# Performance work log

Hardware: AMD Instinct MI355X
Metric: run time of the kernel (lower is better)

The kernel has to match this reference:

```python
import jax, jax.numpy as jnp
import numpy as np

B, T, H, W = 8, 10, 128, 128
WIDTH, NL = 64, 4
MT, MH, MW = 4, 8, 8
H_PRED = 5
MIN_STD = 1e-4


def setup_inputs() -> dict:
    key = jax.random.key(0)
    ks = jax.random.split(key, 12)
    scale = 1.0 / (WIDTH * WIDTH)
    return {
        "frames": jax.random.uniform(ks[0], (B, T, H, W), dtype=jnp.float32),
        "times": jax.random.uniform(ks[1], (B, T), dtype=jnp.float32),
        # lift: Conv3d(c_in=2 -> width, k=1)
        "lift_w": jax.random.normal(ks[2], (WIDTH, 2), dtype=jnp.float32) * 0.5,
        "lift_b": jnp.zeros((WIDTH,), jnp.float32),
        # spectral weights: (layer, quadrant, in, out, mt, mh, mw, re/im)
        "spec_w": jax.random.uniform(ks[3], (NL, 4, WIDTH, WIDTH, MT, MH, MW, 2), dtype=jnp.float32) * scale,
        # skip 1x1 Conv3d per layer
        "skip_w": jax.random.normal(ks[4], (NL, WIDTH, WIDTH), dtype=jnp.float32) * (1.0 / np.sqrt(WIDTH)),
        "skip_b": jnp.zeros((NL, WIDTH), jnp.float32),
        # temporal aggregation Conv3d kernel (h_ctx,1,1): (out, in, T)
        "agg_w": jax.random.normal(ks[5], (WIDTH, WIDTH, T), dtype=jnp.float32) * (1.0 / np.sqrt(WIDTH * T)),
        "agg_b": jnp.zeros((WIDTH,), jnp.float32),
        "fc1_w": jax.random.normal(ks[6], (WIDTH + 2, 128), dtype=jnp.float32) * (1.0 / np.sqrt(WIDTH + 2)),
        "fc1_b": jnp.zeros((128,), jnp.float32),
        "fc2_w": jax.random.normal(ks[7], (128, 2 * H_PRED), dtype=jnp.float32) * (1.0 / np.sqrt(128)),
        "fc2_b": jnp.zeros((2 * H_PRED,), jnp.float32),
    }


def _spectral_conv(x, wl):
    # x: (B, C, T, H, W); wl: (4, C, C, MT, MH, MW, 2) real/imag
    w = wl[..., 0] + 1j * wl[..., 1]  # (4, C, C, MT, MH, MW) complex
    x_ft = jnp.fft.rfftn(x, axes=(-3, -2, -1), norm="ortho")  # (B,C,T,H,W//2+1)
    Bc, C, Tt, Hh, Wf = x_ft.shape

    def mul(blk, wq):
        return jnp.einsum("bixyz,ioxyz->boxyz", blk, wq)

    out_ft = jnp.zeros((Bc, C, Tt, Hh, Wf), dtype=x_ft.dtype)
    out_ft = out_ft.at[:, :, :MT, :MH, :MW].set(mul(x_ft[:, :, :MT, :MH, :MW], w[0]))
    out_ft = out_ft.at[:, :, :MT, Hh - MH:, :MW].set(mul(x_ft[:, :, :MT, Hh - MH:, :MW], w[1]))
    out_ft = out_ft.at[:, :, Tt - MT:, :MH, :MW].set(mul(x_ft[:, :, Tt - MT:, :MH, :MW], w[2]))
    out_ft = out_ft.at[:, :, Tt - MT:, Hh - MH:, :MW].set(mul(x_ft[:, :, Tt - MT:, Hh - MH:, :MW], w[3]))
    return jnp.fft.irfftn(out_ft, s=(Tt, x.shape[-2], x.shape[-1]), axes=(-3, -2, -1), norm="ortho")


def reference(frames, times, lift_w, lift_b, spec_w, skip_w, skip_b,
              agg_w, agg_b, fc1_w, fc1_b, fc2_w, fc2_b):
    gelu = lambda v: jax.nn.gelu(v, approximate=False)
    # feature volume: (B, 2, T, H, W) = [frames, broadcast times]
    t_feat = jnp.broadcast_to(times[:, None, :, None, None], (B, 1, T, H, W))
    feat = jnp.concatenate([frames[:, None], t_feat], axis=1)
    # lift (1x1x1 conv)
    x = jnp.einsum("bcthw,oc->bothw", feat, lift_w) + lift_b[None, :, None, None, None]
    for l in range(NL):
        sx = _spectral_conv(x, spec_w[l])
        sk = jnp.einsum("bithw,oi->bothw", x, skip_w[l]) + skip_b[l][None, :, None, None, None]
        x = gelu(sx + sk)
    # temporal aggregation: valid conv over full T -> (B, C, H, W)
    x = jnp.einsum("bithw,oit->bohw", x, agg_w) + agg_b[None, :, None, None]
    # (x, y) grid channels
    gx = jnp.broadcast_to(jnp.linspace(-1.0, 1.0, W)[None, :], (H, W))
    gy = jnp.broadcast_to(jnp.linspace(-1.0, 1.0, H)[:, None], (H, W))
    grid = jnp.broadcast_to(jnp.stack([gx, gy], 0)[None], (B, 2, H, W))
    x = jnp.concatenate([x, grid], axis=1)  # (B, C+2, H, W)
    x = jnp.transpose(x, (0, 2, 3, 1))      # (B, H, W, C+2)
    x = gelu(x @ fc1_w + fc1_b)
    out = x @ fc2_w + fc2_b                 # (B, H, W, 2*h_pred)
    mu = out[..., 0::2]
    sigma = jax.nn.softplus(out[..., 1::2]) + MIN_STD
    return jnp.concatenate([mu, sigma], axis=-1)  # (B, H, W, 2*h_pred)
```

## Files before the change

### kernel.cpp

```cpp
#include <hip/hip_runtime.h>
#include <math.h>


#define TWO_PI 6.2831853071795864769f
#define ORTHO_SC 2.4705294220065465e-3f

typedef unsigned short u16;
typedef _Float16 f16;
typedef __attribute__((ext_vector_type(8))) _Float16 f16x8;
typedef __attribute__((ext_vector_type(4))) float f32x4;

#define MFMAH(acc, a, b) acc = __builtin_amdgcn_mfma_f32_16x16x32_f16(a, b, acc, 0, 0, 0)

__device__ __forceinline__ u16 f16b(float v) {
  f16 h = (f16)v;
  return __builtin_bit_cast(u16, h);
}
__device__ __forceinline__ float f16lo(float v) {
  f16 h = (f16)v;
  return v - (float)h;
}
__device__ __forceinline__ float f16f(u16 b) {
  return (float)__builtin_bit_cast(f16, b);
}
__device__ __forceinline__ float gelu_fast(float x) {
  float u = 0.7978845608f * (x + 0.044715f * x * x * x);
  float a = fminf(u * 2.885390082f, 30.0f);
  float e = __builtin_exp2f(a);
  return x * e * __builtin_amdgcn_rcpf(e + 1.0f);
}

__global__ __launch_bounds__(256) void k_prep2(const float* __restrict__ skip_w,
                                               const float* __restrict__ agg_w,
                                               u16* __restrict__ swf,
                                               u16* __restrict__ awf,
                                               u16* __restrict__ Tt,
                                               float2* __restrict__ twf,
                                               u16* __restrict__ Ef) {
  int e = blockIdx.x*256 + threadIdx.x;
  if (e < 32768) {
    int j = e & 7, lane = (e >> 3) & 63, half = (e >> 9) & 1, ks = (e >> 10) & 1;
    int strip = (e >> 11) & 3, layer = e >> 13;
    int co = strip*16 + (lane & 15);
    int ci = ks*32 + (lane >> 4)*8 + j;
    float v = skip_w[((size_t)(layer*64) + co)*64 + ci];
    swf[e] = half ? f16b(f16lo(v)) : f16b(v);
  } else if (e < 114688) {
    int ee = e - 32768;
    int j = ee & 7, lane = (ee >> 3) & 63;
    int v9 = ee >> 9;
    int half = v9 & 1; v9 >>= 1;
    int ks = v9 & 1; v9 >>= 1;
    int t = v9 % 10, strip = v9 / 10;
    int co = strip*16 + (lane & 15);
    int ci = ks*32 + (lane >> 4)*8 + j;
    float v = agg_w[((size_t)co*64 + ci)*10 + t];
    awf[ee] = half ? f16b(f16lo(v)) : f16b(v);
  } else if (e < 122880) {
    int ee = e - 114688;
    int half = ee >> 12, r = ee & 4095, w = r >> 5, kk = r & 31;
    int m = kk >> 1;
    float val;
    if (kk >= 16) val = 0.f;
    else if (kk == 0) val = 1.f;
    else if (kk == 1) val = 0.f;
    else {
      float th = TWO_PI * (float)m * (float)w / 128.0f;
      val = (kk & 1) ? (-2.f*sinf(th)) : (2.f*cosf(th));
    }
    Tt[ee] = half ? f16b(f16lo(val)) : f16b(val);
  } else if (e < 123904) {
    int ee = e - 122880;
    int w = ee >> 3, k = ee & 7;
    float th = TWO_PI * (float)k * (float)w / 128.0f;
    twf[ee] = make_float2(cosf(th), -sinf(th));
  } else if (e < 125952) {
    int ee = e - 123904;
    int j = ee & 7, lane = (ee >> 3) & 63, kc = ee >> 9;
    int n = lane & 15, g = lane >> 4;
    int w = kc*32 + g*8 + j;
    int k = n >> 1;
    float th = TWO_PI * (float)k * (float)w / 128.0f;
    float val = (n & 1) ? (-sinf(th)) : cosf(th);
    Ef[ee] = f16b(val);
    Ef[2048 + ee] = f16b(f16lo(val));
  }
}

__global__ __launch_bounds__(128) void k_lift_fwdW(const float* __restrict__ frames,
                                                   const float* __restrict__ times,
                                                   const float* __restrict__ lift_w,
                                                   const float* __restrict__ lift_b,
                                                   const float2* __restrict__ twf,
                                                   u16* __restrict__ xT,
                                                   u16* __restrict__ xw16) {
  __shared__ u16 xs[64][130];
  __shared__ float2 tws[128][8];
  __shared__ float fr[128];
  __shared__ float lw0[64], lw1a[64];
  int bth = blockIdx.x;
  int h = bth & 127; int bt = bth >> 7; int t = bt % 10, b = bt / 10;
  int tid = threadIdx.x;
  for (int i = tid; i < 1024; i += 128) tws[i >> 3][i & 7] = twf[i];
  float tv = times[b*10 + t];
  fr[tid] = frames[((size_t)(b*10 + t)*128 + h)*128 + tid];
  if (tid < 64) { lw0[tid] = lift_w[2*tid]; lw1a[tid] = lift_w[2*tid+1]*tv + lift_b[tid]; }
  __syncthreads();
  {
    int w = tid;
    float f = fr[w];
    unsigned pk[32];
    #pragma unroll
    for (int q = 0; q < 32; ++q) {
      float v0 = f*lw0[2*q] + lw1a[2*q];
      float v1 = f*lw0[2*q+1] + lw1a[2*q+1];
      u16 h0 = f16b(v0), h1 = f16b(v1);
      xs[2*q][w] = h0; xs[2*q+1][w] = h1;
      pk[q] = (unsigned)h0 | ((unsigned)h1 << 16);
    }
    uint4* d4 = (uint4*)(xT + (size_t)bth*8192 + w*64);
    #pragma unroll
    for (int q = 0; q < 8; ++q)
      d4[q] = make_uint4(pk[4*q], pk[4*q+1], pk[4*q+2], pk[4*q+3]);
  }
  __syncthreads();
  {
    int lane = tid & 63, wv = tid >> 6;
    float ar[4] = {0,0,0,0}, ai[4] = {0,0,0,0};
    for (int w2 = 0; w2 < 128; ++w2) {
      float xu = f16f(xs[lane][w2]);
      #pragma unroll
      for (int kk = 0; kk < 4; ++kk) {
        float2 ew = tws[w2][wv*4 + kk];
        ar[kk] += xu*ew.x; ai[kk] += xu*ew.y;
      }
    }
    size_t row = ((size_t)(b*64 + lane)*10 + t)*128 + h;
    unsigned p0 = (unsigned)f16b(ar[0]) | ((unsigned)f16b(ai[0]) << 16);
    unsigned p1 = (unsigned)f16b(ar[1]) | ((unsigned)f16b(ai[1]) << 16);
    unsigned p2 = (unsigned)f16b(ar[2]) | ((unsigned)f16b(ai[2]) << 16);
    unsigned p3 = (unsigned)f16b(ar[3]) | ((unsigned)f16b(ai[3]) << 16);
    *(uint4*)(xw16 + row*16 + wv*8) = make_uint4(p0, p1, p2, p3);
  }
}

__global__ __launch_bounds__(256) void k_fwdHT(const unsigned* __restrict__ xw32,
                                               float2* __restrict__ xf) {
  __shared__ unsigned tile[2][1024];
  __shared__ float2 parts1[1024];
  __shared__ float2 tw128[128];
  int bc = blockIdx.x;
  int b = bc >> 6, c = bc & 63;
  int tid = threadIdx.x;
  if (tid < 128) {
    float s, co; sincosf(TWO_PI * (float)tid / 128.0f, &s, &co);
    tw128[tid] = make_float2(co, -s);
  }
  int tpar = tid >> 7, j = tid & 127;
  int khi = j >> 3, kwi = j & 7;
  int kh = (khi < 8) ? khi : (112 + khi);
  float accr[8], acci[8];
  #pragma unroll
  for (int k = 0; k < 8; ++k) { accr[k] = 0.f; acci[k] = 0.f; }
  for (int tt = 0; tt < 5; ++tt) {
    __syncthreads();
    for (int u = tid; u < 2048; u += 256) {
      int tg = u >> 10, idx = u & 1023;
      tile[tg][idx] = xw32[((size_t)bc*10 + tg*5 + tt)*1024 + idx];
    }
    __syncthreads();
    float xr = 0.f, xi = 0.f;
    for (int h = 0; h < 128; ++h) {
      unsigned uv = tile[tpar][h*8 + kwi];
      float vx = f16f((u16)uv);
      float vy = f16f((u16)(uv >> 16));
      float2 tw = tw128[(h*kh) & 127];
      xr += vx*tw.x - vy*tw.y;
      xi += vx*tw.y + vy*tw.x;
    }
    int t = tpar*5 + tt;
    float sb, cb; sincosf(TWO_PI * (float)t / 10.0f, &sb, &cb);
    float p_r[10], p_i[10];
    p_r[0] = 1.f; p_i[0] = 0.f; p_r[1] = cb; p_i[1] = -sb;
    #pragma unroll
    for (int k = 2; k < 10; ++k) {
      p_r[k] = p_r[k-1]*p_r[1] - p_i[k-1]*p_i[1];
      p_i[k] = p_r[k-1]*p_i[1] + p_i[k-1]*p_r[1];
    }
    #pragma unroll
    for (int kti = 0; kti < 8; ++kti) {
      int kt = (kti < 4) ? kti : kti + 2;
      accr[kti] += xr*p_r[kt] - xi*p_i[kt];
      acci[kti] += xr*p_i[kt] + xi*p_r[kt];
    }
  }
  __syncthreads();
  if (tpar == 1) {
    #pragma unroll
    for (int kti = 0; kti < 8; ++kti)
      parts1[j*8 + kti] = make_float2(accr[kti], acci[kti]);
  }
  __syncthreads();
  if (tpar == 0) {
    #pragma unroll
    for (int kti = 0; kti < 8; ++kti) {
      float2 bq = parts1[j*8 + kti];
      xf[((size_t)b*1024 + kti*128 + j)*64 + c] =
          make_float2((accr[kti] + bq.x)*ORTHO_SC, (acci[kti] + bq.y)*ORTHO_SC);
    }
  }
}

__global__ __launch_bounds__(256) void k_mix(const float2* __restrict__ xf,
                                             const float* __restrict__ spec_w_l,
                                             float2* __restrict__ yf) {
  __shared__ float2 xfs[8][4][64];
  int m0 = blockIdx.x * 4;
  for (int i = threadIdx.x; i < 2048; i += 256) {
    int bb = i >> 8, mi = (i >> 6) & 3, ci = i & 63;
    xfs[bb][mi][ci] = xf[((size_t)bb*1024 + m0 + mi)*64 + ci];
  }
  __syncthreads();
  int co = threadIdx.x & 63, mi = threadIdx.x >> 6;
  int m = m0 + mi;
  int kti = m >> 7, khi = (m >> 3) & 15, kwi = m & 7;
  int q = ((kti >= 4) ? 2 : 0) + ((khi >= 8) ? 1 : 0);
  int modeidx = ((kti & 3)*8 + (khi & 7))*8 + kwi;
  const float2* wp = (const float2*)spec_w_l
                     + ((size_t)(q*64)*64 + co)*256 + modeidx;
  float accr[8], acci[8];
  #pragma unroll
  for (int bb = 0; bb < 8; ++bb) { accr[bb] = 0.f; acci[bb] = 0.f; }
  for (int ci = 0; ci < 64; ++ci) {
    float2 wv = wp[(size_t)ci*16384];
    #pragma unroll
    for (int bb = 0; bb < 8; ++bb) {
      float2 xv = xfs[bb][mi][ci];
      accr[bb] += xv.x*wv.x - xv.y*wv.y;
      acci[bb] += xv.x*wv.y + xv.y*wv.x;
    }
  }
  #pragma unroll
  for (int bb = 0; bb < 8; ++bb)
    yf[((size_t)bb*64 + co)*1024 + m] = make_float2(accr[bb], acci[bb]);
}

__global__ __launch_bounds__(256) void k_invTH(const float2* __restrict__ yf,
                                               unsigned* __restrict__ zh16) {
  __shared__ float2 ybuf[1024];
  __shared__ float2 ztb[2][128];
  __shared__ float2 tw128[128];
  int bc = blockIdx.x;
  int b = bc >> 6, c = bc & 63;
  int tid = threadIdx.x;
  for (int u = tid; u < 1024; u += 256) ybuf[u] = yf[(size_t)bc*1024 + u];
  if (tid < 128) {
    float s, co; sincosf(TWO_PI * (float)tid / 128.0f, &s, &co);
    tw128[tid] = make_float2(co, s);
  }
  int tpar = tid >> 7, j = tid & 127;
  __syncthreads();
  for (int tt = 0; tt < 5; ++tt) {
    int t = tt*2 + tpar;
    {
      float sb, cb; sincosf(TWO_PI * (float)t / 10.0f, &sb, &cb);
      float p_r[10], p_i[10];
      p_r[0] = 1.f; p_i[0] = 0.f; p_r[1] = cb; p_i[1] = sb;
      #pragma unroll
      for (int k = 2; k < 10; ++k) {
        p_r[k] = p_r[k-1]*p_r[1] - p_i[k-1]*p_i[1];
        p_i[k] = p_r[k-1]*p_i[1] + p_i[k-1]*p_r[1];
      }
      float zr = 0.f, zi = 0.f;
      #pragma unroll
      for (int kti = 0; kti < 8; ++kti) {
        int kt = (kti < 4) ? kti : kti + 2;
        float2 v = ybuf[kti*128 + j];
        zr += v.x*p_r[kt] - v.y*p_i[kt];
        zi += v.x*p_i[kt] + v.y*p_r[kt];
      }
      ztb[tpar][j] = make_float2(zr*ORTHO_SC, zi*ORTHO_SC);
    }
    __syncthreads();
    {
      int h = j;
      float ar[8], ai[8];
      #pragma unroll
      for (int kw = 0; kw < 8; ++kw) { ar[kw] = 0.f; ai[kw] = 0.f; }
      #pragma unroll
      for (int khi = 0; khi < 16; ++khi) {
        int kh = (khi < 8) ? khi : (112 + khi);
        float2 tw = tw128[(h*kh) & 127];
        #pragma unroll
        for (int kw = 0; kw < 8; ++kw) {
          float2 v = ztb[tpar][khi*8 + kw];
          ar[kw] += v.x*tw.x - v.y*tw.y;
          ai[kw] += v.x*tw.y + v.y*tw.x;
        }
      }
      unsigned* dst = zh16 + (((size_t)(b*10 + t)*128 + h)*64 + c)*8;
      #pragma unroll
      for (int kw = 0; kw < 8; ++kw)
        dst[kw] = (unsigned)f16b(ar[kw]) | ((unsigned)f16b(ai[kw]) << 16);
    }
    __syncthreads();
  }
}

__global__ __launch_bounds__(256, 4) void k_invW_mfma(const u16* __restrict__ xTin,
                                                      const unsigned* __restrict__ zh16,
                                                      const u16* __restrict__ swf_l,
                                                      const u16* __restrict__ Tt,
                                                      const u16* __restrict__ Ef,
                                                      const float* __restrict__ skb,
                                                      u16* __restrict__ xTo,
                                                      u16* __restrict__ xw16,
                                                      int do_dft) {
  __shared__ __align__(16) char smem[20480];
  u16* B = (u16*)smem;
  u16* zAh = (u16*)(smem + 18432);
  int tid = threadIdx.x;
  int bth = blockIdx.x;
  int lane = tid & 63;
  int wq = tid >> 6;
  int cL = lane & 15;
  int g = lane >> 4;

  f16x8 Th[2], Tl[2];
  #pragma unroll
  for (int t2 = 0; t2 < 2; ++t2) {
    int wrow = wq*32 + t2*16 + cL;
    Th[t2] = *(const f16x8*)(Tt + wrow*32 + g*8);
    Tl[t2] = *(const f16x8*)(Tt + 4096 + wrow*32 + g*8);
  }
  {
    const uint4* xsrc = (const uint4*)(xTin + (size_t)bth*8192);
    for (int u = tid; u < 1024; u += 256) {
      int w = u >> 3, c = u & 7;
      ((uint4*)(B + w*72))[c] = xsrc[u];
    }
  }
  {
    const unsigned* zsrc = zh16 + (size_t)bth*512;
    for (int u = tid; u < 512; u += 256) {
      int co = u >> 3, m = u & 7;
      *(unsigned*)(zAh + co*16 + 2*m) = zsrc[u];
    }
  }
  __syncthreads();

  f32x4 acc[4][2];
  #pragma unroll
  for (int s = 0; s < 4; ++s)
    #pragma unroll
    for (int t2 = 0; t2 < 2; ++t2) acc[s][t2] = (f32x4){0.f,0.f,0.f,0.f};

  #pragma unroll
  for (int kb = 0; kb < 2; ++kb) {
    f16x8 Ah[4], Al[4];
    #pragma unroll
    for (int s = 0; s < 4; ++s) {
      Ah[s] = *(const f16x8*)(swf_l + (size_t)(s*2048 + kb*1024 + lane*8));
      Al[s] = *(const f16x8*)(swf_l + (size_t)(s*2048 + kb*1024 + 512 + lane*8));
    }
    #pragma unroll
    for (int t2 = 0; t2 < 2; ++t2) {
      int wrow = wq*32 + t2*16 + cL;
      f16x8 bh = *(const f16x8*)(B + wrow*72 + kb*32 + g*8);
      #pragma unroll
      for (int s = 0; s < 4; ++s) {
        MFMAH(acc[s][t2], Ah[s], bh);
        MFMAH(acc[s][t2], Al[s], bh);
      }
    }
  }
  {
    f16x8 Azh[4];
    f16x8 zero8 = {0,0,0,0,0,0,0,0};
    #pragma unroll
    for (int s = 0; s < 4; ++s)
      Azh[s] = (g < 2) ? *(const f16x8*)(zAh + (s*16 + cL)*16 + g*8) : zero8;
    #pragma unroll
    for (int t2 = 0; t2 < 2; ++t2) {
      #pragma unroll
      for (int s = 0; s < 4; ++s) {
        MFMAH(acc[s][t2], Azh[s], Th[t2]);
        MFMAH(acc[s][t2], Azh[s], Tl[t2]);
      }
    }
  }

  __syncthreads();
  unsigned* out32 = (unsigned*)smem;
  #pragma unroll
  for (int s = 0; s < 4; ++s) {
    float4 b4 = *(const float4*)(skb + s*16 + g*4);
    float bb[4] = {b4.x, b4.y, b4.z, b4.w};
    #pragma unroll
    for (int t2 = 0; t2 < 2; ++t2) {
      int w = wq*32 + t2*16 + cL;
      u16 gb[4];
      #pragma unroll
      for (int r = 0; r < 4; ++r) {
        float val = acc[s][t2][r] + bb[r];
        gb[r] = f16b(gelu_fast(val));
      }
      out32[(s*8 + g*2 + 0)*130 + w] = (unsigned)gb[0] | ((unsigned)gb[1] << 16);
      out32[(s*8 + g*2 + 1)*130 + w] = (unsigned)gb[2] | ((unsigned)gb[3] << 16);
    }
  }
  __syncthreads();
  {
    uint4* xdst = (uint4*)(xTo + (size_t)bth*8192);
    for (int u = tid; u < 1024; u += 256) {
      int w = u >> 3, c = u & 7;
      unsigned r0 = out32[(c*4 + 0)*130 + w];
      unsigned r1 = out32[(c*4 + 1)*130 + w];
      unsigned r2 = out32[(c*4 + 2)*130 + w];
      unsigned r3 = out32[(c*4 + 3)*130 + w];
      xdst[u] = make_uint4(r0, r1, r2, r3);
    }
  }
  if (do_dft) {
    f32x4 acc2 = (f32x4){0.f,0.f,0.f,0.f};
    int row = wq*8 + (cL >> 1);
    int sh = (cL & 1) * 16;
    #pragma unroll
    for (int kc = 0; kc < 4; ++kc) {
      const unsigned* p = out32 + row*130 + kc*32 + g*8;
      uint2 d0 = *(const uint2*)(p);
      uint2 d1 = *(const uint2*)(p + 2);
      uint2 d2 = *(const uint2*)(p + 4);
      uint2 d3 = *(const uint2*)(p + 6);
      f16x8 a;
      a[0] = __builtin_bit_cast(f16, (u16)(d0.x >> sh));
      a[1] = __builtin_bit_cast(f16, (u16)(d0.y >> sh));
      a[2] = __builtin_bit_cast(f16, (u16)(d1.x >> sh));
      a[3] = __builtin_bit_cast(f16, (u16)(d1.y >> sh));
      a[4] = __builtin_bit_cast(f16, (u16)(d2.x >> sh));
      a[5] = __builtin_bit_cast(f16, (u16)(d2.y >> sh));
      a[6] = __builtin_bit_cast(f16, (u16)(d3.x >> sh));
      a[7] = __builtin_bit_cast(f16, (u16)(d3.y >> sh));
      f16x8 eh = *(const f16x8*)(Ef + (kc*64 + lane)*8);
      f16x8 el = *(const f16x8*)(Ef + 2048 + (kc*64 + lane)*8);
      MFMAH(acc2, a, eh);
      MFMAH(acc2, a, el);
    }
    int h = bth & 127; int bt = bth >> 7; int t = bt % 10, b = bt / 10;
    #pragma unroll
    for (int r = 0; r < 4; ++r) {
      int co = wq*16 + g*4 + r;
      size_t row2 = ((size_t)(b*64 + co)*10 + t)*128 + h;
      xw16[row2*16 + cL] = f16b(acc2[r]);
    }
  }
}

__global__ __launch_bounds__(256) void k_agg_head(const u16* __restrict__ xT,
                                                  const u16* __restrict__ awf,
                                                  const float* __restrict__ agg_b,
                                                  const float* __restrict__ fc1_w,
                                                  const float* __restrict__ fc1_b,
                                                  const float* __restrict__ fc2_w,
                                                  const float* __restrict__ fc2_b,
                                                  float* __restrict__ out) {
  __shared__ __align__(16) char smem[43520];
  u16* B = (u16*)smem;
  float* outx = (float*)smem;
  float* part = (float*)(smem + 33280);
  float* w2s  = (float*)(smem + 38400);
  int tid = threadIdx.x;
  int bid = blockIdx.x;
  int h = bid & 127, b = bid >> 7;
  int lane = tid & 63;
  int wq = tid >> 6;
  int cL = lane & 15;
  int g = lane >> 4;
  for (int i = tid; i < 1280; i += 256) w2s[i] = fc2_w[i];

  f32x4 acc[4][2];
  #pragma unroll
  for (int s = 0; s < 4; ++s)
    #pragma unroll
    for (int t2 = 0; t2 < 2; ++t2) acc[s][t2] = (f32x4){0.f,0.f,0.f,0.f};

  for (int t = 0; t < 10; ++t) {
    __syncthreads();
    {
      const uint4* xsrc = (const uint4*)(xT + ((size_t)(b*10 + t)*128 + h)*8192);
      for (int u = tid; u < 1024; u += 256) {
        int w = u >> 3, c = u & 7;
        ((uint4*)(B + w*72))[c] = xsrc[u];
      }
    }
    __syncthreads();
    #pragma unroll
    for (int kc = 0; kc < 2; ++kc) {
      f16x8 Ah[4], Al[4];
      #pragma unroll
      for (int s = 0; s < 4; ++s) {
        const u16* af = awf + (size_t)((s*10 + t)*4 + kc*2)*512;
        Ah[s] = *(const f16x8*)(af + lane*8);
        Al[s] = *(const f16x8*)(af + 512 + lane*8);
      }
      #pragma unroll
      for (int t2 = 0; t2 < 2; ++t2) {
        int wrow = wq*32 + t2*16 + cL;
        f16x8 bh = *(const f16x8*)(B + wrow*72 + kc*32 + g*8);
        #pragma unroll
        for (int s = 0; s < 4; ++s) {
          MFMAH(acc[s][t2], Ah[s], bh);
          MFMAH(acc[s][t2], Al[s], bh);
        }
      }
    }
  }

  __syncthreads();
  #pragma unroll
  for (int s = 0; s < 4; ++s) {
    float4 b4 = *(const float4*)(agg_b + s*16 + g*4);
    float bb[4] = {b4.x, b4.y, b4.z, b4.w};
    #pragma unroll
    for (int t2 = 0; t2 < 2; ++t2) {
      int w = wq*32 + t2*16 + cL;
      #pragma unroll
      for (int r = 0; r < 4; ++r) {
        int co = s*16 + g*4 + r;
        outx[co*130 + w] = acc[s][t2][r] + bb[r];
      }
    }
  }
  __syncthreads();

  {
    int w = tid & 127, oh = tid >> 7;
    float v[64];
    #pragma unroll
    for (int c = 0; c < 64; ++c) v[c] = outx[c*130 + w];
    float gx = -1.f + 2.f*(float)w/127.f;
    float gy = -1.f + 2.f*(float)h/127.f;
    float o2[10];
    #pragma unroll
    for (int j = 0; j < 10; ++j) o2[j] = 0.f;
    int o0 = oh*64;
    for (int o = o0; o < o0 + 64; ++o) {
      float a = fc1_b[o];
      #pragma unroll
      for (int i = 0; i < 64; ++i) a += v[i]*fc1_w[i*128 + o];
      a += gx*fc1_w[64*128 + o] + gy*fc1_w[65*128 + o];
      float gl = gelu_fast(a);
      #pragma unroll
      for (int j = 0; j < 10; ++j) o2[j] += gl*w2s[o*10 + j];
    }
    if (oh) {
      #pragma unroll
      for (int j = 0; j < 10; ++j) part[w*10 + j] = o2[j];
    }
    __syncthreads();
    if (!oh) {
      float tot[10];
      #pragma unroll
      for (int j = 0; j < 10; ++j) tot[j] = o2[j] + part[w*10 + j] + fc2_b[j];
      float* dst = out + ((size_t)bid*128 + w)*10;
      #pragma unroll
      for (int k = 0; k < 5; ++k) dst[k] = tot[2*k];
      #pragma unroll
      for (int k = 0; k < 5; ++k) {
        float sv = tot[2*k+1];
        float sp = fmaxf(sv, 0.f) + log1pf(expf(-fabsf(sv)));
        dst[5 + k] = sp + 1e-4f;
      }
    }
  }
}

extern "C" void kernel_launch(void* const* d_in, const int* in_sizes, int n_in,
                              void* d_out, int out_size, void* d_ws, size_t ws_size,
                              hipStream_t stream) {
  const float* frames = (const float*)d_in[0];
  const float* times  = (const float*)d_in[1];
  const float* lift_w = (const float*)d_in[2];
  const float* lift_b = (const float*)d_in[3];
  const float* spec_w = (const float*)d_in[4];
  const float* skip_w = (const float*)d_in[5];
  const float* skip_b = (const float*)d_in[6];
  const float* agg_w  = (const float*)d_in[7];
  const float* agg_b  = (const float*)d_in[8];
  const float* fc1_w  = (const float*)d_in[9];
  const float* fc1_b  = (const float*)d_in[10];
  const float* fc2_w  = (const float*)d_in[11];
  const float* fc2_b  = (const float*)d_in[12];
  float* out = (float*)d_out;
  char* ws = (char*)d_ws;

  size_t off = 0;
  u16*      xT  = (u16*)(ws + off);      off += (size_t)10240*8192*2;
  u16*      xw16= (u16*)(ws + off);      off += (size_t)655360*16*2;
  float2*   xf  = (float2*)(ws + off);   off += (size_t)8*1024*64*8;
  float2*   yf  = (float2*)(ws + off);   off += (size_t)8*1024*64*8;
  unsigned* zh16= (unsigned*)(ws + off); off += (size_t)10240*512*4;
  u16*      swf = (u16*)(ws + off);      off += (size_t)32768*2;
  u16*      awf = (u16*)(ws + off);      off += (size_t)81920*2;
  u16*      Tt  = (u16*)(ws + off);      off += (size_t)8192*2;
  float2*   twf = (float2*)(ws + off);   off += (size_t)1024*8;
  u16*      Ef  = (u16*)(ws + off);      off += (size_t)4096*2;

  k_prep2<<<492, 256, 0, stream>>>(skip_w, agg_w, swf, awf, Tt, twf, Ef);
  k_lift_fwdW<<<10240, 128, 0, stream>>>(frames, times, lift_w, lift_b, twf, xT, xw16);

  for (int l = 0; l < 4; ++l) {
    k_fwdHT<<<512, 256, 0, stream>>>((const unsigned*)xw16, xf);
    k_mix<<<256, 256, 0, stream>>>(xf, spec_w + (size_t)l*4*64*64*256*2, yf);
    k_invTH<<<512, 256, 0, stream>>>(yf, zh16);
    k_invW_mfma<<<10240, 256, 0, stream>>>(xT, zh16, swf + (size_t)l*8192, Tt, Ef,
                                           skip_b + l*64, xT, xw16, (l < 3) ? 1 : 0);
  }
  k_agg_head<<<1024, 256, 0, stream>>>(xT, awf, agg_b, fc1_w, fc1_b, fc2_w, fc2_b, out);
}
```

Baseline: 1.059 ms.

## Split aggregation and head, run fc1 on MFMA with packed fp16 weights

Splits the fused aggregation+MLP head kernel in two. The aggregation result now goes to a global fp32 buffer, and a new head kernel computes fc1 with split-fp16 (hi/lo) MFMA. The fc1 weights and bias, with the bias folded in as an extra input column, are pre-packed in the prep kernel, and the grid coordinates are built in a swizzled LDS tile. This replaces the scalar per-thread 64x128 fc1 loop with matrix-core work. The cost is an extra global round trip of the aggregated activations (about 33 MB) and one more launch. The activations are also rounded to fp16 only, with no lo part, which lowers precision.

```diff
diff --git a/kernel.cpp b/kernel.cpp
--- a/kernel.cpp
+++ b/kernel.cpp
@@ -32,11 +32,14 @@
 
 __global__ __launch_bounds__(256) void k_prep2(const float* __restrict__ skip_w,
                                                const float* __restrict__ agg_w,
+                                               const float* __restrict__ fc1_w,
+                                               const float* __restrict__ fc1_b,
                                                u16* __restrict__ swf,
                                                u16* __restrict__ awf,
                                                u16* __restrict__ Tt,
                                                float2* __restrict__ twf,
-                                               u16* __restrict__ Ef) {
+                                               u16* __restrict__ Ef,
+                                               u16* __restrict__ f1f) {
   int e = blockIdx.x*256 + threadIdx.x;
   if (e < 32768) {
     int j = e & 7, lane = (e >> 3) & 63, half = (e >> 9) & 1, ks = (e >> 10) & 1;
@@ -84,6 +87,18 @@
     float val = (n & 1) ? (-sinf(th)) : cosf(th);
     Ef[ee] = f16b(val);
     Ef[2048 + ee] = f16b(f16lo(val));
+  } else if (e < 150528) {
+    int ee = e - 125952;
+    int j = ee & 7, lane = (ee >> 3) & 63, hl = (ee >> 9) & 1;
+    int rest = ee >> 10;
+    int kc = rest % 3, strip = rest / 3;
+    int o = strip*16 + (lane & 15);
+    int k = kc*32 + (lane >> 4)*8 + j;
+    float v;
+    if (k < 66) v = fc1_w[(size_t)k*128 + o];
+    else if (k == 66) v = fc1_b[o];
+    else v = 0.f;
+    f1f[ee] = hl ? f16b(f16lo(v)) : f16b(v);
   }
 }
 
@@ -456,19 +471,11 @@
   }
 }
 
-__global__ __launch_bounds__(256) void k_agg_head(const u16* __restrict__ xT,
+__global__ __launch_bounds__(256) void k_agg_mfma(const u16* __restrict__ xT,
                                                   const u16* __restrict__ awf,
                                                   const float* __restrict__ agg_b,
-                                                  const float* __restrict__ fc1_w,
-                                                  const float* __restrict__ fc1_b,
-                                                  const float* __restrict__ fc2_w,
-                                                  const float* __restrict__ fc2_b,
-                                                  float* __restrict__ out) {
-  __shared__ __align__(16) char smem[43520];
-  u16* B = (u16*)smem;
-  float* outx = (float*)smem;
-  float* part = (float*)(smem + 33280);
-  float* w2s  = (float*)(smem + 38400);
+                                                  float* __restrict__ xa) {
+  __shared__ __align__(16) u16 B[128*72];
   int tid = threadIdx.x;
   int bid = blockIdx.x;
   int h = bid & 127, b = bid >> 7;
@@ -476,7 +483,6 @@
   int wq = tid >> 6;
   int cL = lane & 15;
   int g = lane >> 4;
-  for (int i = tid; i < 1280; i += 256) w2s[i] = fc2_w[i];
 
   f32x4 acc[4][2];
   #pragma unroll
@@ -516,7 +522,6 @@
     }
   }
 
-  __syncthreads();
   #pragma unroll
   for (int s = 0; s < 4; ++s) {
     float4 b4 = *(const float4*)(agg_b + s*16 + g*4);
@@ -527,42 +532,113 @@
       #pragma unroll
       for (int r = 0; r < 4; ++r) {
         int co = s*16 + g*4 + r;
-        outx[co*130 + w] = acc[s][t2][r] + bb[r];
-      }
-    }
-  }
-  __syncthreads();
-
-  {
-    int w = tid & 127, oh = tid >> 7;
-    float v[64];
-    #pragma unroll
-    for (int c = 0; c < 64; ++c) v[c] = outx[c*130 + w];
-    float gx = -1.f + 2.f*(float)w/127.f;
-    float gy = -1.f + 2.f*(float)h/127.f;
-    float o2[10];
-    #pragma unroll
-    for (int j = 0; j < 10; ++j) o2[j] = 0.f;
-    int o0 = oh*64;
-    for (int o = o0; o < o0 + 64; ++o) {
-      float a = fc1_b[o];
-      #pragma unroll
-      for (int i = 0; i < 64; ++i) a += v[i]*fc1_w[i*128 + o];
-      a += gx*fc1_w[64*128 + o] + gy*fc1_w[65*128 + o];
-      float gl = gelu_fast(a);
-      #pragma unroll
-      for (int j = 0; j < 10; ++j) o2[j] += gl*w2s[o*10 + j];
-    }
-    if (oh) {
-      #pragma unroll
-      for (int j = 0; j < 10; ++j) part[w*10 + j] = o2[j];
-    }
-    __syncthreads();
-    if (!oh) {
+        xa[((size_t)(b*64 + co)*128 + h)*128 + w] = acc[s][t2][r] + bb[r];
+      }
+    }
+  }
+}
+
+__global__ __launch_bounds__(256) void k_head_mfma(const float* __restrict__ xa,
+                                                   const u16* __restrict__ f1f,
+                                                   const float* __restrict__ fc2_w,
+                                                   const float* __restrict__ fc2_b,
+                                                   float* __restrict__ out) {
+  __shared__ __align__(16) u16 B[128*128];
+  __shared__ float w2s[1280];
+  int tid = threadIdx.x;
+  int bid = blockIdx.x;
+  int h = bid & 127, b = bid >> 7;
+  for (int i = tid; i < 1280; i += 256) w2s[i] = fc2_w[i];
+  for (int u = tid; u < 2048; u += 256) {
+    int co = u >> 5, w4 = u & 31;
+    float4 v = *(const float4*)(xa + ((size_t)(b*64 + co)*128 + h)*128 + w4*4);
+    float vv[4] = {v.x, v.y, v.z, v.w};
+    int kg = co >> 3, kj = co & 7;
+    #pragma unroll
+    for (int jj = 0; jj < 4; ++jj) {
+      int w = w4*4 + jj;
+      B[w*128 + ((kg ^ (w & 7)) << 3) + kj] = f16b(vv[jj]);
+    }
+  }
+  for (int u = tid; u < 512; u += 256) {
+    int w = u & 127, kgo = u >> 7;
+    int kg = 8 + kgo;
+    u16* dst = &B[w*128 + ((kg ^ (w & 7)) << 3)];
+    if (kgo == 0) {
+      float gx = -1.f + 2.f*(float)w/127.f;
+      float gy = -1.f + 2.f*(float)h/127.f;
+      dst[0] = f16b(gx); dst[1] = f16b(gy); dst[2] = f16b(1.f);
+      dst[3] = 0; dst[4] = 0; dst[5] = 0; dst[6] = 0; dst[7] = 0;
+    } else {
+      #pragma unroll
+      for (int q = 0; q < 8; ++q) dst[q] = 0;
+    }
+  }
+  __syncthreads();
+
+  int lane = tid & 63, wq = tid >> 6, cL = lane & 15, g = lane >> 4;
+  f32x4 acc[8][2];
+  #pragma unroll
+  for (int s = 0; s < 8; ++s)
+    #pragma unroll
+    for (int t2 = 0; t2 < 2; ++t2) acc[s][t2] = (f32x4){0.f,0.f,0.f,0.f};
+
+  #pragma unroll
+  for (int kc = 0; kc < 3; ++kc) {
+    f16x8 bfr[2];
+    #pragma unroll
+    for (int t2 = 0; t2 < 2; ++t2) {
+      int wrow = wq*32 + t2*16 + cL;
+      int kg = kc*4 + g;
+      bfr[t2] = *(const f16x8*)(&B[wrow*128 + ((kg ^ (wrow & 7)) << 3)]);
+    }
+    #pragma unroll
+    for (int s = 0; s < 8; ++s) {
+      f16x8 Ah = *(const f16x8*)(f1f + (size_t)(((s*3 + kc)*2 + 0)*64 + lane)*8);
+      f16x8 Al = *(const f16x8*)(f1f + (size_t)(((s*3 + kc)*2 + 1)*64 + lane)*8);
+      #pragma unroll
+      for (int t2 = 0; t2 < 2; ++t2) {
+        MFMAH(acc[s][t2], Ah, bfr[t2]);
+        MFMAH(acc[s][t2], Al, bfr[t2]);
+      }
+    }
+  }
+
+  float o2[2][10];
+  #pragma unroll
+  for (int t2 = 0; t2 < 2; ++t2)
+    #pragma unroll
+    for (int j = 0; j < 10; ++j) o2[t2][j] = 0.f;
+  #pragma unroll
+  for (int s = 0; s < 8; ++s) {
+    #pragma unroll
+    for (int t2 = 0; t2 < 2; ++t2) {
+      #pragma unroll
+      for (int r = 0; r < 4; ++r) {
+        int o = s*16 + g*4 + r;
+        float gl = gelu_fast(acc[s][t2][r]);
+        #pragma unroll
+        for (int j = 0; j < 10; ++j) o2[t2][j] += gl * w2s[o*10 + j];
+      }
+    }
+  }
+  #pragma unroll
+  for (int t2 = 0; t2 < 2; ++t2)
+    #pragma unroll
+    for (int j = 0; j < 10; ++j) {
+      float v = o2[t2][j];
+      v += __shfl_xor(v, 16, 64);
+      v += __shfl_xor(v, 32, 64);
+      o2[t2][j] = v;
+    }
+  if (g == 0) {
+    #pragma unroll
+    for (int t2 = 0; t2 < 2; ++t2) {
+      int w = wq*32 + t2*16 + cL;
+      float* dst = out + ((size_t)bid*128 + w)*10;
       float tot[10];
       #pragma unroll
-      for (int j = 0; j < 10; ++j) tot[j] = o2[j] + part[w*10 + j] + fc2_b[j];
-      float* dst = out + ((size_t)bid*128 + w)*10;
+      for (int j = 0; j < 10; ++j) tot[j] = o2[t2][j] + fc2_b[j];
       #pragma unroll
       for (int k = 0; k < 5; ++k) dst[k] = tot[2*k];
       #pragma unroll
@@ -600,13 +676,16 @@
   float2*   xf  = (float2*)(ws + off);   off += (size_t)8*1024*64*8;
   float2*   yf  = (float2*)(ws + off);   off += (size_t)8*1024*64*8;
   unsigned* zh16= (unsigned*)(ws + off); off += (size_t)10240*512*4;
+  float*    xa  = (float*)(ws + off);    off += (size_t)8*64*128*128*4;
   u16*      swf = (u16*)(ws + off);      off += (size_t)32768*2;
   u16*      awf = (u16*)(ws + off);      off += (size_t)81920*2;
   u16*      Tt  = (u16*)(ws + off);      off += (size_t)8192*2;
   float2*   twf = (float2*)(ws + off);   off += (size_t)1024*8;
   u16*      Ef  = (u16*)(ws + off);      off += (size_t)4096*2;
-
-  k_prep2<<<492, 256, 0, stream>>>(skip_w, agg_w, swf, awf, Tt, twf, Ef);
+  u16*      f1f = (u16*)(ws + off);      off += (size_t)24576*2;
+
+  k_prep2<<<588, 256, 0, stream>>>(skip_w, agg_w, fc1_w, fc1_b,
+                                   swf, awf, Tt, twf, Ef, f1f);
   k_lift_fwdW<<<10240, 128, 0, stream>>>(frames, times, lift_w, lift_b, twf, xT, xw16);
 
   for (int l = 0; l < 4; ++l) {
@@ -616,5 +695,6 @@
     k_invW_mfma<<<10240, 256, 0, stream>>>(xT, zh16, swf + (size_t)l*8192, Tt, Ef,
                                            skip_b + l*64, xT, xw16, (l < 3) ? 1 : 0);
   }
-  k_agg_head<<<1024, 256, 0, stream>>>(xT, awf, agg_b, fc1_w, fc1_b, fc2_w, fc2_b, out);
-}
+  k_agg_mfma<<<1024, 256, 0, stream>>>(xT, awf, agg_b, xa);
+  k_head_mfma<<<1024, 256, 0, stream>>>(xa, f1f, fc2_w, fc2_b, out);
+}
```

New measurement: 949.8 us (median of 2 runs). -10.3%, faster.
